# Optimization experiments

Measured on AMD Instinct MI355X. Metric: run time of the kernel, lower is better.

The kernel has to match this reference:

```python
import jax, jax.numpy as jnp
import numpy as np

BETA = 0.1  # sliced_fgw_distance default (forward does not override it)
EPS = 1e-12  # F.normalize eps


def setup_inputs() -> dict:
    key = jax.random.key(0)
    k1, k2, k3 = jax.random.split(key, 3)
    N, D, P = 2048, 512, 10
    z = jax.random.normal(k1, (N, D), dtype=jnp.float32)
    gmm_noise = jax.random.normal(k2, (N, D), dtype=jnp.float32)
    projections = jax.random.normal(k3, (D, P), dtype=jnp.float32)
    return {"z": z, "gmm_noise": gmm_noise, "projections": projections}


def _pairwise_sq_diff(a):
    # a: [N, P] -> [N, N, P] of (a_i - a_j)^2  (p=2, so abs()**2 == square)
    return (a[:, None, :] - a[None, :, :]) ** 2


def reference(z, gmm_noise, projections):
    # gmm_samples = F.normalize(randn_like(z)) : L2-normalize rows
    norm = jnp.maximum(jnp.linalg.norm(gmm_noise, axis=1, keepdims=True), EPS)
    gmm_samples = gmm_noise / norm  # [N, D]

    post = jnp.sort(z @ projections, axis=0)            # [N, P] ascending
    prior_proj = gmm_samples @ projections              # [N, P]
    prior1 = jnp.sort(prior_proj, axis=0)               # ascending
    prior2 = prior1[::-1]                               # descending sort

    post_diff = _pairwise_sq_diff(post)                 # [N, N, P]
    gw1 = jnp.mean((post_diff - _pairwise_sq_diff(prior1)) ** 2, axis=(0, 1))  # [P]
    gw2 = jnp.mean((post_diff - _pairwise_sq_diff(prior2)) ** 2, axis=(0, 1))  # [P]

    w1 = jnp.sum((post - prior1) ** 2, axis=0)          # [P]
    w2 = jnp.sum((post - prior2) ** 2, axis=0)          # [P]

    fgw1 = (1.0 - BETA) * w1 + BETA * gw1
    fgw2 = (1.0 - BETA) * w2 + BETA * gw2
    return jnp.mean(jnp.minimum(fgw1, fgw2))
```

## Files before the change

### kernel.cpp

```cpp
#include <hip/hip_runtime.h>
#include <math.h>

#define N_ROWS 2048
#define D_DIM 512
#define P_DIM 10

__device__ inline float wave_reduce_f(float v) {
#pragma unroll
  for (int off = 32; off > 0; off >>= 1) v += __shfl_down(v, off, 64);
  return v;
}

__device__ inline double wave_reduce_d(double v) {
#pragma unroll
  for (int off = 32; off > 0; off >>= 1) v += __shfl_down(v, off, 64);
  return v;
}

__global__ __launch_bounds__(256) void rc_proj_kernel(
    const float* __restrict__ z, const float* __restrict__ g,
    const float* __restrict__ proj, float* __restrict__ post_cm,
    float* __restrict__ prior_cm) {
  __shared__ float pl[P_DIM * D_DIM];
  for (int i = threadIdx.x; i < P_DIM * D_DIM; i += 256) {
    int k = i / P_DIM, p = i - k * P_DIM;
    pl[p * D_DIM + k] = proj[i];
  }
  __syncthreads();
  const int wave = threadIdx.x >> 6, lane = threadIdx.x & 63;
  const int row = blockIdx.x * 4 + wave;
  const float* zr = z + (size_t)row * D_DIM;
  const float* gr = g + (size_t)row * D_DIM;
  float zv[8], gv[8];
#pragma unroll
  for (int m = 0; m < 8; ++m) {
    zv[m] = zr[m * 64 + lane];
    gv[m] = gr[m * 64 + lane];
  }
  float n2 = 0.f;
#pragma unroll
  for (int m = 0; m < 8; ++m) n2 += gv[m] * gv[m];
  float az[P_DIM], ag[P_DIM];
#pragma unroll
  for (int p = 0; p < P_DIM; ++p) { az[p] = 0.f; ag[p] = 0.f; }
#pragma unroll
  for (int m = 0; m < 8; ++m) {
#pragma unroll
    for (int p = 0; p < P_DIM; ++p) {
      float w = pl[p * D_DIM + m * 64 + lane];
      az[p] += zv[m] * w;
      ag[p] += gv[m] * w;
    }
  }
#pragma unroll
  for (int p = 0; p < P_DIM; ++p) {
    az[p] = wave_reduce_f(az[p]);
    ag[p] = wave_reduce_f(ag[p]);
  }
  n2 = wave_reduce_f(n2);
  if (lane == 0) {
    float inv = 1.f / fmaxf(sqrtf(n2), 1e-12f);
    for (int p = 0; p < P_DIM; ++p) {
      post_cm[p * N_ROWS + row] = az[p];
      prior_cm[p * N_ROWS + row] = ag[p] * inv;
    }
  }
}

__global__ __launch_bounds__(1024) void rc_sort_kernel(
    float* __restrict__ post_cm, float* __restrict__ prior_cm) {
  float* buf = (blockIdx.x < P_DIM) ? post_cm + blockIdx.x * N_ROWS
                                    : prior_cm + (blockIdx.x - P_DIM) * N_ROWS;
  __shared__ float s[N_ROWS];
  const int tid = threadIdx.x;
  s[tid] = buf[tid];
  s[tid + 1024] = buf[tid + 1024];
  for (unsigned k = 2; k <= N_ROWS; k <<= 1) {
    for (unsigned j = k >> 1; j > 0; j >>= 1) {
      __syncthreads();
#pragma unroll
      for (int t = 0; t < 2; ++t) {
        unsigned idx = (unsigned)tid + (unsigned)t * 1024u;
        unsigned ixj = idx ^ j;
        if (ixj > idx) {
          float x = s[idx], y = s[ixj];
          bool up = (idx & k) == 0;
          if (up ? (x > y) : (x < y)) { s[idx] = y; s[ixj] = x; }
        }
      }
    }
  }
  __syncthreads();
  buf[tid] = s[tid];
  buf[tid + 1024] = s[tid + 1024];
}

__global__ __launch_bounds__(256) void rc_stats_kernel(
    const float* __restrict__ post_cm, const float* __restrict__ prior_cm,
    float* __restrict__ fgw) {
  const int p = blockIdx.x % P_DIM;
  const int variant = blockIdx.x / P_DIM;
  const float* a = post_cm + p * N_ROWS;
  const float* b = prior_cm + p * N_ROWS;
  double S[10];
#pragma unroll
  for (int t = 0; t < 10; ++t) S[t] = 0.0;
  for (int i = threadIdx.x; i < N_ROWS; i += 256) {
    double av = (double)a[i];
    double bv = (double)(variant ? b[N_ROWS - 1 - i] : b[i]);
    double a2 = av * av, b2 = bv * bv;
    double s = a2 - b2;
    S[0] += s * s;
    S[1] += s;
    S[2] += s * av;
    S[3] += av;
    S[4] += s * bv;
    S[5] += bv;
    S[6] += a2;
    S[7] += av * bv;
    S[8] += b2;
    double d = av - bv;
    S[9] += d * d;
  }
#pragma unroll
  for (int t = 0; t < 10; ++t) S[t] = wave_reduce_d(S[t]);
  __shared__ double sm[4][10];
  const int wave = threadIdx.x >> 6, lane = threadIdx.x & 63;
  if (lane == 0) {
#pragma unroll
    for (int t = 0; t < 10; ++t) sm[wave][t] = S[t];
  }
  __syncthreads();
  if (threadIdx.x == 0) {
    double T[10];
#pragma unroll
    for (int t = 0; t < 10; ++t)
      T[t] = sm[0][t] + sm[1][t] + sm[2][t] + sm[3][t];
    const double nn = (double)N_ROWS;
    double gw = (2.0 * nn * T[0] + 2.0 * T[1] * T[1]
                 - 8.0 * (T[2] * T[3] - T[4] * T[5])
                 + 4.0 * (T[6] * T[6] - 2.0 * T[7] * T[7] + T[8] * T[8]))
                / (nn * nn);
    double w = T[9];
    fgw[blockIdx.x] = (float)(0.9 * w + 0.1 * gw);
  }
}

__global__ void rc_final_kernel(const float* __restrict__ fgw,
                                float* __restrict__ out) {
  if (threadIdx.x == 0 && blockIdx.x == 0) {
    float s = 0.f;
    for (int p = 0; p < P_DIM; ++p) s += fminf(fgw[p], fgw[P_DIM + p]);
    out[0] = s * (1.f / P_DIM);
  }
}

extern "C" void kernel_launch(void* const* d_in, const int* in_sizes, int n_in,
                              void* d_out, int out_size, void* d_ws,
                              size_t ws_size, hipStream_t stream) {
  const float* z = (const float*)d_in[0];
  const float* g = (const float*)d_in[1];
  const float* proj = (const float*)d_in[2];
  float* out = (float*)d_out;
  float* post_cm = (float*)d_ws;
  float* prior_cm = post_cm + N_ROWS * P_DIM;
  float* fgw = prior_cm + N_ROWS * P_DIM;

  rc_proj_kernel<<<N_ROWS / 4, 256, 0, stream>>>(z, g, proj, post_cm, prior_cm);
  rc_sort_kernel<<<2 * P_DIM, 1024, 0, stream>>>(post_cm, prior_cm);
  rc_stats_kernel<<<2 * P_DIM, 256, 0, stream>>>(post_cm, prior_cm, fgw);
  rc_final_kernel<<<1, 64, 0, stream>>>(fgw, out);
}
```

Measured before the change: 94.85 us.

## Fuse bitonic sort with stats using register and shuffle sorting

Merges the sort and stats kernels into one block per projection that sorts both the post and prior columns in registers. Compare-exchange steps with stride up to 32 use wave shuffles, the 1024 stride is done in-thread, and other strides go through double-buffered LDS with a single barrier per step. Both sort orders' statistics are then computed in one pass, with the descending variant read as a reversal from LDS. This removes a kernel launch, a global round trip and most barriers and LDS traffic of the old sort. In exchange, each block carries twice the sorting work and the grid shrinks to ten blocks.

```diff
diff --git a/kernel.cpp b/kernel.cpp
--- a/kernel.cpp
+++ b/kernel.cpp
@@ -67,82 +67,142 @@
   }
 }
 
-__global__ __launch_bounds__(1024) void rc_sort_kernel(
-    float* __restrict__ post_cm, float* __restrict__ prior_cm) {
-  float* buf = (blockIdx.x < P_DIM) ? post_cm + blockIdx.x * N_ROWS
-                                    : prior_cm + (blockIdx.x - P_DIM) * N_ROWS;
-  __shared__ float s[N_ROWS];
-  const int tid = threadIdx.x;
-  s[tid] = buf[tid];
-  s[tid + 1024] = buf[tid + 1024];
-  for (unsigned k = 2; k <= N_ROWS; k <<= 1) {
-    for (unsigned j = k >> 1; j > 0; j >>= 1) {
-      __syncthreads();
-#pragma unroll
-      for (int t = 0; t < 2; ++t) {
-        unsigned idx = (unsigned)tid + (unsigned)t * 1024u;
-        unsigned ixj = idx ^ j;
-        if (ixj > idx) {
-          float x = s[idx], y = s[ixj];
-          bool up = (idx & k) == 0;
-          if (up ? (x > y) : (x < y)) { s[idx] = y; s[ixj] = x; }
-        }
-      }
-    }
-  }
-  __syncthreads();
-  buf[tid] = s[tid];
-  buf[tid + 1024] = s[tid + 1024];
-}
-
-__global__ __launch_bounds__(256) void rc_stats_kernel(
+__global__ __launch_bounds__(1024) void rc_sortstats_kernel(
     const float* __restrict__ post_cm, const float* __restrict__ prior_cm,
     float* __restrict__ fgw) {
-  const int p = blockIdx.x % P_DIM;
-  const int variant = blockIdx.x / P_DIM;
-  const float* a = post_cm + p * N_ROWS;
-  const float* b = prior_cm + p * N_ROWS;
-  double S[10];
-#pragma unroll
-  for (int t = 0; t < 10; ++t) S[t] = 0.0;
-  for (int i = threadIdx.x; i < N_ROWS; i += 256) {
-    double av = (double)a[i];
-    double bv = (double)(variant ? b[N_ROWS - 1 - i] : b[i]);
-    double a2 = av * av, b2 = bv * bv;
-    double s = a2 - b2;
-    S[0] += s * s;
-    S[1] += s;
-    S[2] += s * av;
-    S[3] += av;
-    S[4] += s * bv;
-    S[5] += bv;
-    S[6] += a2;
-    S[7] += av * bv;
-    S[8] += b2;
-    double d = av - bv;
-    S[9] += d * d;
-  }
-#pragma unroll
-  for (int t = 0; t < 10; ++t) S[t] = wave_reduce_d(S[t]);
-  __shared__ double sm[4][10];
-  const int wave = threadIdx.x >> 6, lane = threadIdx.x & 63;
+  const int p = blockIdx.x;
+  const int tid = threadIdx.x;
+  const int lane = tid & 63;
+  __shared__ float sA[2][N_ROWS];
+  __shared__ float sB[2][N_ROWS];
+  __shared__ double smd[16][14];
+
+  float a0 = post_cm[p * N_ROWS + tid];
+  float a1 = post_cm[p * N_ROWS + tid + 1024];
+  float b0 = prior_cm[p * N_ROWS + tid];
+  float b1 = prior_cm[p * N_ROWS + tid + 1024];
+  int cb = 0;
+
+  auto shfl_phase = [&](unsigned j, unsigned k) {
+    bool lo = ((lane & (int)j) == 0);
+    bool up0 = ((tid & (int)k) == 0);
+    bool up1 = (((tid + 1024) & (int)k) == 0);
+    float t;
+    t = __shfl_xor(a0, (int)j, 64);
+    a0 = (lo == up0) ? fminf(a0, t) : fmaxf(a0, t);
+    t = __shfl_xor(a1, (int)j, 64);
+    a1 = (lo == up1) ? fminf(a1, t) : fmaxf(a1, t);
+    t = __shfl_xor(b0, (int)j, 64);
+    b0 = (lo == up0) ? fminf(b0, t) : fmaxf(b0, t);
+    t = __shfl_xor(b1, (int)j, 64);
+    b1 = (lo == up1) ? fminf(b1, t) : fmaxf(b1, t);
+  };
+
+  auto lds_phase = [&](unsigned j, unsigned k) {
+    float* A = sA[cb];
+    float* B = sB[cb];
+    A[tid] = a0;
+    A[tid + 1024] = a1;
+    B[tid] = b0;
+    B[tid + 1024] = b1;
+    __syncthreads();
+    unsigned i0 = (unsigned)tid, i1 = (unsigned)tid + 1024u;
+    float qa0 = A[i0 ^ j], qa1 = A[i1 ^ j];
+    float qb0 = B[i0 ^ j], qb1 = B[i1 ^ j];
+    bool lo0 = ((i0 & j) == 0), lo1 = ((i1 & j) == 0);
+    bool up0 = ((i0 & k) == 0), up1 = ((i1 & k) == 0);
+    a0 = (lo0 == up0) ? fminf(a0, qa0) : fmaxf(a0, qa0);
+    a1 = (lo1 == up1) ? fminf(a1, qa1) : fmaxf(a1, qa1);
+    b0 = (lo0 == up0) ? fminf(b0, qb0) : fmaxf(b0, qb0);
+    b1 = (lo1 == up1) ? fminf(b1, qb1) : fmaxf(b1, qb1);
+    cb ^= 1;
+  };
+
+#pragma unroll
+  for (unsigned k = 2; k <= 64; k <<= 1)
+#pragma unroll
+    for (unsigned j = k >> 1; j >= 1; j >>= 1) shfl_phase(j, k);
+#pragma unroll
+  for (unsigned k = 128; k <= 2048; k <<= 1) {
+#pragma unroll
+    for (unsigned j = k >> 1; j >= 64; j >>= 1) {
+      if (j == 1024) {
+        float na = fminf(a0, a1);
+        a1 = fmaxf(a0, a1);
+        a0 = na;
+        float nb = fminf(b0, b1);
+        b1 = fmaxf(b0, b1);
+        b0 = nb;
+      } else {
+        lds_phase(j, k);
+      }
+    }
+#pragma unroll
+    for (unsigned j = 32; j >= 1; j >>= 1) shfl_phase(j, k);
+  }
+
+  __syncthreads();
+  float* Bs = sB[0];
+  Bs[tid] = b0;
+  Bs[tid + 1024] = b1;
+  __syncthreads();
+  float br0 = Bs[2047 - tid];
+  float br1 = Bs[1023 - tid];
+
+  double S[14];
+  {
+    double av0 = a0, av1 = a1, bv0 = b0, bv1 = b1, bw0 = br0, bw1 = br1;
+    double a20 = av0 * av0, a21 = av1 * av1;
+    double b20 = bv0 * bv0, b21 = bv1 * bv1;
+    double c20 = bw0 * bw0, c21 = bw1 * bw1;
+    double s10 = a20 - b20, s11 = a21 - b21;
+    double s20 = a20 - c20, s21 = a21 - c21;
+    S[0] = av0 + av1;
+    S[1] = bv0 + bv1;
+    S[2] = a20 + a21;
+    S[3] = b20 + b21;
+    S[4] = s10 * s10 + s11 * s11;
+    S[5] = s10 * av0 + s11 * av1;
+    S[6] = s10 * bv0 + s11 * bv1;
+    S[7] = av0 * bv0 + av1 * bv1;
+    double d10 = av0 - bv0, d11 = av1 - bv1;
+    S[8] = d10 * d10 + d11 * d11;
+    S[9] = s20 * s20 + s21 * s21;
+    S[10] = s20 * av0 + s21 * av1;
+    S[11] = s20 * bw0 + s21 * bw1;
+    S[12] = av0 * bw0 + av1 * bw1;
+    double d20 = av0 - bw0, d21 = av1 - bw1;
+    S[13] = d20 * d20 + d21 * d21;
+  }
+#pragma unroll
+  for (int t = 0; t < 14; ++t) S[t] = wave_reduce_d(S[t]);
+  const int wv = tid >> 6;
   if (lane == 0) {
 #pragma unroll
-    for (int t = 0; t < 10; ++t) sm[wave][t] = S[t];
-  }
-  __syncthreads();
-  if (threadIdx.x == 0) {
-    double T[10];
-#pragma unroll
-    for (int t = 0; t < 10; ++t)
-      T[t] = sm[0][t] + sm[1][t] + sm[2][t] + sm[3][t];
+    for (int t = 0; t < 14; ++t) smd[wv][t] = S[t];
+  }
+  __syncthreads();
+  if (tid == 0) {
+    double T[14];
+#pragma unroll
+    for (int t = 0; t < 14; ++t) {
+      double acc = 0.0;
+      for (int w = 0; w < 16; ++w) acc += smd[w][t];
+      T[t] = acc;
+    }
     const double nn = (double)N_ROWS;
-    double gw = (2.0 * nn * T[0] + 2.0 * T[1] * T[1]
-                 - 8.0 * (T[2] * T[3] - T[4] * T[5])
-                 + 4.0 * (T[6] * T[6] - 2.0 * T[7] * T[7] + T[8] * T[8]))
-                / (nn * nn);
-    double w = T[9];
-    fgw[blockIdx.x] = (float)(0.9 * w + 0.1 * gw);
+    double Ss = T[2] - T[3];
+    double gw1 = (2.0 * nn * T[4] + 2.0 * Ss * Ss -
+                  8.0 * (T[5] * T[0] - T[6] * T[1]) +
+                  4.0 * (T[2] * T[2] - 2.0 * T[7] * T[7] + T[3] * T[3])) /
+                 (nn * nn);
+    double gw2 = (2.0 * nn * T[9] + 2.0 * Ss * Ss -
+                  8.0 * (T[10] * T[0] - T[11] * T[1]) +
+                  4.0 * (T[2] * T[2] - 2.0 * T[12] * T[12] + T[3] * T[3])) /
+                 (nn * nn);
+    double f1 = 0.9 * T[8] + 0.1 * gw1;
+    double f2 = 0.9 * T[13] + 0.1 * gw2;
+    fgw[p] = (float)fmin(f1, f2);
   }
 }
 
@@ -150,7 +210,7 @@
                                 float* __restrict__ out) {
   if (threadIdx.x == 0 && blockIdx.x == 0) {
     float s = 0.f;
-    for (int p = 0; p < P_DIM; ++p) s += fminf(fgw[p], fgw[P_DIM + p]);
+    for (int p = 0; p < P_DIM; ++p) s += fgw[p];
     out[0] = s * (1.f / P_DIM);
   }
 }
@@ -166,8 +226,8 @@
   float* prior_cm = post_cm + N_ROWS * P_DIM;
   float* fgw = prior_cm + N_ROWS * P_DIM;
 
-  rc_proj_kernel<<<N_ROWS / 4, 256, 0, stream>>>(z, g, proj, post_cm, prior_cm);
-  rc_sort_kernel<<<2 * P_DIM, 1024, 0, stream>>>(post_cm, prior_cm);
-  rc_stats_kernel<<<2 * P_DIM, 256, 0, stream>>>(post_cm, prior_cm, fgw);
+  rc_proj_kernel<<<N_ROWS / 4, 256, 0, stream>>>(z, g, proj, post_cm,
+                                                 prior_cm);
+  rc_sortstats_kernel<<<P_DIM, 1024, 0, stream>>>(post_cm, prior_cm, fgw);
   rc_final_kernel<<<1, 64, 0, stream>>>(fgw, out);
 }
```

After: 89.22 us. -5.9%, faster.

## Replace bitonic sort with parallel rank-by-counting using index-tagged sort keys

Applied to the files above, without the earlier changes.

The per-column bitonic sort (one 1024-thread block per column, many barrier stages) is replaced by a counting-rank kernel. Each element compares its packed (order-preserving key, row index) against every element of its column and scatters to its rank. Packing the row index makes the keys unique, so ranks form a permutation. This spreads the work over many more blocks and removes barriers, at the cost of quadratic comparisons and doubled workspace for 64-bit keys.

```diff
diff --git a/kernel.cpp b/kernel.cpp
--- a/kernel.cpp
+++ b/kernel.cpp
@@ -17,10 +17,15 @@
   return v;
 }
 
+__device__ inline unsigned f32_sortkey(float v) {
+  unsigned u = __float_as_uint(v);
+  return (u & 0x80000000u) ? ~u : (u | 0x80000000u);
+}
+
 __global__ __launch_bounds__(256) void rc_proj_kernel(
     const float* __restrict__ z, const float* __restrict__ g,
-    const float* __restrict__ proj, float* __restrict__ post_cm,
-    float* __restrict__ prior_cm) {
+    const float* __restrict__ proj, unsigned long long* __restrict__ post_key,
+    unsigned long long* __restrict__ prior_key) {
   __shared__ float pl[P_DIM * D_DIM];
   for (int i = threadIdx.x; i < P_DIM * D_DIM; i += 256) {
     int k = i / P_DIM, p = i - k * P_DIM;
@@ -61,47 +66,43 @@
   if (lane == 0) {
     float inv = 1.f / fmaxf(sqrtf(n2), 1e-12f);
     for (int p = 0; p < P_DIM; ++p) {
-      post_cm[p * N_ROWS + row] = az[p];
-      prior_cm[p * N_ROWS + row] = ag[p] * inv;
+      post_key[p * N_ROWS + row] =
+          ((unsigned long long)f32_sortkey(az[p]) << 32) | (unsigned)row;
+      prior_key[p * N_ROWS + row] =
+          ((unsigned long long)f32_sortkey(ag[p] * inv) << 32) | (unsigned)row;
     }
   }
 }
 
-__global__ __launch_bounds__(1024) void rc_sort_kernel(
-    float* __restrict__ post_cm, float* __restrict__ prior_cm) {
-  float* buf = (blockIdx.x < P_DIM) ? post_cm + blockIdx.x * N_ROWS
-                                    : prior_cm + (blockIdx.x - P_DIM) * N_ROWS;
-  __shared__ float s[N_ROWS];
-  const int tid = threadIdx.x;
-  s[tid] = buf[tid];
-  s[tid + 1024] = buf[tid + 1024];
-  for (unsigned k = 2; k <= N_ROWS; k <<= 1) {
-    for (unsigned j = k >> 1; j > 0; j >>= 1) {
-      __syncthreads();
-#pragma unroll
-      for (int t = 0; t < 2; ++t) {
-        unsigned idx = (unsigned)tid + (unsigned)t * 1024u;
-        unsigned ixj = idx ^ j;
-        if (ixj > idx) {
-          float x = s[idx], y = s[ixj];
-          bool up = (idx & k) == 0;
-          if (up ? (x > y) : (x < y)) { s[idx] = y; s[ixj] = x; }
-        }
-      }
-    }
+__global__ __launch_bounds__(256) void rc_rank_kernel(
+    const unsigned long long* __restrict__ keys,
+    float* __restrict__ sorted) {
+  const int c = blockIdx.x >> 3;
+  const int chunk = blockIdx.x & 7;
+  const unsigned long long* kcol = keys + (size_t)c * N_ROWS;
+  const int i = chunk * 256 + threadIdx.x;
+  const unsigned long long myk = kcol[i];
+  int r0 = 0, r1 = 0, r2 = 0, r3 = 0;
+#pragma unroll 16
+  for (int j = 0; j < N_ROWS; j += 4) {
+    r0 += (kcol[j + 0] < myk) ? 1 : 0;
+    r1 += (kcol[j + 1] < myk) ? 1 : 0;
+    r2 += (kcol[j + 2] < myk) ? 1 : 0;
+    r3 += (kcol[j + 3] < myk) ? 1 : 0;
   }
-  __syncthreads();
-  buf[tid] = s[tid];
-  buf[tid + 1024] = s[tid + 1024];
+  const int rank = r0 + r1 + r2 + r3;
+  unsigned u = (unsigned)(myk >> 32);
+  float v = __uint_as_float((u & 0x80000000u) ? (u & 0x7FFFFFFFu) : ~u);
+  sorted[(size_t)c * N_ROWS + rank] = v;
 }
 
 __global__ __launch_bounds__(256) void rc_stats_kernel(
-    const float* __restrict__ post_cm, const float* __restrict__ prior_cm,
+    const float* __restrict__ post_s, const float* __restrict__ prior_s,
     float* __restrict__ fgw) {
   const int p = blockIdx.x % P_DIM;
   const int variant = blockIdx.x / P_DIM;
-  const float* a = post_cm + p * N_ROWS;
-  const float* b = prior_cm + p * N_ROWS;
+  const float* a = post_s + p * N_ROWS;
+  const float* b = prior_s + p * N_ROWS;
   double S[10];
 #pragma unroll
   for (int t = 0; t < 10; ++t) S[t] = 0.0;
@@ -162,12 +163,16 @@
   const float* g = (const float*)d_in[1];
   const float* proj = (const float*)d_in[2];
   float* out = (float*)d_out;
-  float* post_cm = (float*)d_ws;
-  float* prior_cm = post_cm + N_ROWS * P_DIM;
-  float* fgw = prior_cm + N_ROWS * P_DIM;
+  unsigned long long* post_key = (unsigned long long*)d_ws;
+  unsigned long long* prior_key = post_key + N_ROWS * P_DIM;
+  float* post_s = (float*)(prior_key + N_ROWS * P_DIM);
+  float* prior_s = post_s + N_ROWS * P_DIM;
+  float* fgw = prior_s + N_ROWS * P_DIM;
 
-  rc_proj_kernel<<<N_ROWS / 4, 256, 0, stream>>>(z, g, proj, post_cm, prior_cm);
-  rc_sort_kernel<<<2 * P_DIM, 1024, 0, stream>>>(post_cm, prior_cm);
-  rc_stats_kernel<<<2 * P_DIM, 256, 0, stream>>>(post_cm, prior_cm, fgw);
+  rc_proj_kernel<<<N_ROWS / 4, 256, 0, stream>>>(z, g, proj, post_key,
+                                                 prior_key);
+  rc_rank_kernel<<<2 * P_DIM * (N_ROWS / 256), 256, 0, stream>>>(post_key,
+                                                                 post_s);
+  rc_stats_kernel<<<2 * P_DIM, 256, 0, stream>>>(post_s, prior_s, fgw);
   rc_final_kernel<<<1, 64, 0, stream>>>(fgw, out);
 }
```

New measurement: 113.3 us. +19.4%, slower.
